# Kernel tuning notes

Measured on AMD Instinct MI355X. Metric: run time of the kernel, lower is better.

The kernel has to match this reference:

```python
import jax, jax.numpy as jnp
import numpy as np

B, P, F = 128, 4096, 32
K, D = 8, 64
ITERS = 2
EPS_ATTN = 1e-8
EPS_LN = 1e-5
SCALE = D ** -0.5


def _layernorm(x, g, b):
    mu = jnp.mean(x, axis=-1, keepdims=True)
    var = jnp.mean((x - mu) ** 2, axis=-1, keepdims=True)
    return (x - mu) * jax.lax.rsqrt(var + EPS_LN) * g + b


def setup_inputs() -> dict:
    key = jax.random.key(0)
    ks = jax.random.split(key, 16)
    s = lambda fan_in: 1.0 / np.sqrt(fan_in)
    inp = {
        "x": jax.random.normal(ks[0], (B, P, F), dtype=jnp.float32),
        "noise": jax.random.normal(ks[1], (B, K, D), dtype=jnp.float32),
        "slots_mu": jax.random.normal(ks[2], (1, 1, D), dtype=jnp.float32),
        "slots_sigma": jnp.ones((1, 1, D), dtype=jnp.float32) * 0.1,
        # torch Linear weights: [out, in]
        "Wq": jax.random.uniform(ks[3], (D, D), jnp.float32, -s(D), s(D)),
        "Wk": jax.random.uniform(ks[4], (D, F), jnp.float32, -s(F), s(F)),
        "Wv": jax.random.uniform(ks[5], (D, F), jnp.float32, -s(F), s(F)),
        # GRUCell params: weight_ih/[3D,D], weight_hh/[3D,D], biases [3D]
        "W_ih": jax.random.uniform(ks[6], (3 * D, D), jnp.float32, -s(D), s(D)),
        "W_hh": jax.random.uniform(ks[7], (3 * D, D), jnp.float32, -s(D), s(D)),
        "b_ih": jax.random.uniform(ks[8], (3 * D,), jnp.float32, -s(D), s(D)),
        "b_hh": jax.random.uniform(ks[9], (3 * D,), jnp.float32, -s(D), s(D)),
        "ln_in_g": jnp.ones((F,), jnp.float32),
        "ln_in_b": jnp.zeros((F,), jnp.float32),
        "ln_slots_g": jnp.ones((D,), jnp.float32),
        "ln_slots_b": jnp.zeros((D,), jnp.float32),
        "ff_ln_g": jnp.ones((D,), jnp.float32),
        "ff_ln_b": jnp.zeros((D,), jnp.float32),
        "ff_W1": jax.random.uniform(ks[10], (2 * D, D), jnp.float32, -s(D), s(D)),
        "ff_b1": jax.random.uniform(ks[11], (2 * D,), jnp.float32, -s(D), s(D)),
        "ff_W2": jax.random.uniform(ks[12], (D, 2 * D), jnp.float32, -s(2 * D), s(2 * D)),
        "ff_b2": jax.random.uniform(ks[13], (D,), jnp.float32, -s(2 * D), s(2 * D)),
    }
    return inp


def _gru_cell(x, h, W_ih, W_hh, b_ih, b_hh):
    # x, h: [N, D]
    gi = x @ W_ih.T + b_ih  # [N, 3D]
    gh = h @ W_hh.T + b_hh
    i_r, i_z, i_n = jnp.split(gi, 3, axis=-1)
    h_r, h_z, h_n = jnp.split(gh, 3, axis=-1)
    r = jax.nn.sigmoid(i_r + h_r)
    z = jax.nn.sigmoid(i_z + h_z)
    n = jnp.tanh(i_n + r * h_n)
    return (1.0 - z) * n + z * h


def reference(x, noise, slots_mu, slots_sigma, Wq, Wk, Wv, W_ih, W_hh, b_ih, b_hh,
              ln_in_g, ln_in_b, ln_slots_g, ln_slots_b,
              ff_ln_g, ff_ln_b, ff_W1, ff_b1, ff_W2, ff_b2):
    x_norm = _layernorm(x, ln_in_g, ln_in_b)          # [B,P,F]
    k = x_norm @ Wk.T                                  # [B,P,D]
    v = x_norm @ Wv.T                                  # [B,P,D]
    slots = slots_mu + jnp.abs(slots_sigma) * noise    # [B,K,D]
    last_attn = None
    for _ in range(ITERS):
        slots_prev = slots
        q = _layernorm(slots, ln_slots_g, ln_slots_b) @ Wq.T  # [B,K,D]
        dots = jnp.einsum('bkd,bpd->bkp', q, k) * SCALE       # [B,K,P]
        attn = jax.nn.softmax(dots, axis=1) + EPS_ATTN        # softmax over slots
        attn = attn / jnp.sum(attn, axis=-1, keepdims=True)   # normalize over pixels
        last_attn = attn
        updates = jnp.einsum('bkp,bpd->bkd', attn, v)         # [B,K,D]
        h = _gru_cell(updates.reshape(-1, D), slots_prev.reshape(-1, D),
                      W_ih, W_hh, b_ih, b_hh).reshape(x.shape[0], K, D)
        ff_in = _layernorm(h, ff_ln_g, ff_ln_b)
        ff_out = jax.nn.relu(ff_in @ ff_W1.T + ff_b1) @ ff_W2.T + ff_b2
        slots = h + ff_out
    return slots, last_attn
```

## Files before the change

### kernel.cpp

```cpp
#include <hip/hip_runtime.h>
#include <hip/hip_bf16.h>
#include <stdint.h>

#define Bb 128
#define Pp 4096
#define Ff 32
#define Kk 8
#define Dd 64

constexpr float EPS_ATTN_ = 1e-8f;
constexpr float EPS_LN_   = 1e-5f;
constexpr float SCALE_    = 0.125f;

typedef __attribute__((ext_vector_type(8))) short short8;
typedef __attribute__((ext_vector_type(4))) float floatx4;
typedef __attribute__((ext_vector_type(4))) unsigned uintx4;

__device__ __forceinline__ unsigned short f2bf(float f) {
  union { float f; unsigned u; } c; c.f = f;
  unsigned u = c.u + 0x7fffu + ((c.u >> 16) & 1u);
  return (unsigned short)(u >> 16);
}
__device__ __forceinline__ unsigned pkbf(float a, float b) {
  __hip_bfloat162 h2 = __float22bfloat162_rn(make_float2(a, b));
  union { __hip_bfloat162 h; unsigned u; } c; c.h = h2;
  return c.u;
}
__device__ __forceinline__ float wsum(float v) {
  v += __shfl_xor(v, 1, 64);  v += __shfl_xor(v, 2, 64);
  v += __shfl_xor(v, 4, 64);  v += __shfl_xor(v, 8, 64);
  v += __shfl_xor(v, 16, 64); v += __shfl_xor(v, 32, 64);
  return v;
}

__global__ __launch_bounds__(512) void init_kernel(
    const float* __restrict__ noise, const float* __restrict__ smu,
    const float* __restrict__ ssig, const float* __restrict__ Wq,
    const float* __restrict__ Wk,
    const float* __restrict__ lsg, const float* __restrict__ lsb,
    float* __restrict__ slots, unsigned short* __restrict__ qt_bf,
    float* __restrict__ acc_t, float* __restrict__ accs) {
  const int b = blockIdx.x;
  const int k = threadIdx.x >> 6;
  const int j = threadIdx.x & 63;
  __shared__ float lnv[Kk][Dd];
  __shared__ float wq[64 * 65];
  __shared__ float wk[64 * 33];
  {
    const float4* g4 = (const float4*)Wq;
    #pragma unroll
    for (int i = 0; i < 2; ++i) {
      int f4i = threadIdx.x + i * 512;
      float4 v = g4[f4i];
      int fi = f4i * 4, row = fi >> 6, col = fi & 63;
      float* dst = &wq[row * 65 + col];
      dst[0] = v.x; dst[1] = v.y; dst[2] = v.z; dst[3] = v.w;
    }
    const float4* gk = (const float4*)Wk;
    float4 v = gk[threadIdx.x];
    int fi = threadIdx.x * 4, row = fi >> 5, col = fi & 31;
    float* dst = &wk[row * 33 + col];
    dst[0] = v.x; dst[1] = v.y; dst[2] = v.z; dst[3] = v.w;
  }
  const size_t rk = (size_t)b * Kk + k;
  float s0 = smu[j] + fabsf(ssig[j]) * noise[rk * Dd + j];
  slots[rk * Dd + j] = s0;
  float mu  = wsum(s0) * (1.f / 64.f);
  float dc  = s0 - mu;
  float var = wsum(dc * dc) * (1.f / 64.f);
  float xn  = dc * rsqrtf(var + EPS_LN_) * lsg[j] + lsb[j];
  lnv[k][j] = xn;
  __syncthreads();
  float q = 0.f;
  #pragma unroll 8
  for (int d = 0; d < Dd; ++d) q = fmaf(wq[j * 65 + d], lnv[k][d], q);
  __syncthreads();
  lnv[k][j] = q * SCALE_;
  __syncthreads();
  if (j < Ff) {
    float qt = 0.f;
    #pragma unroll 8
    for (int d = 0; d < Dd; ++d) qt = fmaf(lnv[k][d], wk[d * 33 + j], qt);
    qt_bf[((size_t)b * 16 + k) * Ff + j]     = f2bf(qt);
    qt_bf[((size_t)b * 16 + k + 8) * Ff + j] = 0;
    acc_t[rk * Ff + j] = 0.f;
  }
  if (j == 0) accs[rk] = 0.f;
}

#define ROUNDS 2
template <bool LAST>
__global__ __launch_bounds__(256) void fattn_kernel(
    const float* __restrict__ x, const unsigned short* __restrict__ qt_bf,
    const float* __restrict__ lg, const float* __restrict__ lb,
    float* __restrict__ acc_t, float* __restrict__ accs,
    float* __restrict__ attn_out) {
  const int b  = blockIdx.x;
  const int w    = threadIdx.x >> 6;
  const int lane = threadIdx.x & 63;
  const int m    = lane & 15;
  const int quad = lane >> 4;
  __shared__ __align__(16) unsigned short xb[256 * 40];
  __shared__ __align__(16) unsigned short xbT[32 * 264];
  __shared__ __align__(16) unsigned short A_lds[4][8][72];

  const short8 aq = *(const short8*)(qt_bf + ((size_t)b * 16 + m) * Ff + quad * 8);

  float Ss0 = 0.f, Ss1 = 0.f, Ss2 = 0.f, Ss3 = 0.f;
  floatx4 Cg0 = {0.f,0.f,0.f,0.f}, Cg1 = {0.f,0.f,0.f,0.f};

  for (int rr = 0; rr < ROUNDS; ++rr) {
    const int p0 = (blockIdx.y * ROUNDS + rr) * 256;
    if (rr) __syncthreads();
    const float4* xp = (const float4*)(x + ((size_t)b * Pp + p0 + threadIdx.x) * Ff);
    float4 xr[8];
    #pragma unroll
    for (int i = 0; i < 8; ++i) xr[i] = xp[i];
    unsigned pku[16];
    {
      float xv[Ff];
      #pragma unroll
      for (int i = 0; i < 8; ++i) {
        xv[i*4] = xr[i].x; xv[i*4+1] = xr[i].y; xv[i*4+2] = xr[i].z; xv[i*4+3] = xr[i].w;
      }
      float mu = 0.f;
      #pragma unroll
      for (int j = 0; j < Ff; ++j) mu += xv[j];
      mu *= (1.f / Ff);
      float var = 0.f;
      #pragma unroll
      for (int j = 0; j < Ff; ++j) { float d = xv[j] - mu; var = fmaf(d, d, var); }
      var *= (1.f / Ff);
      float rn = rsqrtf(var + EPS_LN_);
      #pragma unroll
      for (int j = 0; j < Ff; ++j) xv[j] = (xv[j] - mu) * rn * lg[j] + lb[j];
      #pragma unroll
      for (int p = 0; p < 16; ++p) pku[p] = pkbf(xv[2 * p], xv[2 * p + 1]);
    }
    #pragma unroll
    for (int j8 = 0; j8 < 4; ++j8)
      *(uintx4*)&xb[threadIdx.x * 40 + j8 * 8] = *(uintx4*)&pku[j8 * 4];
    #pragma unroll
    for (int p = 0; p < 16; ++p) {
      xbT[(2 * p)     * 264 + threadIdx.x] = (unsigned short)(pku[p] & 0xffffu);
      xbT[(2 * p + 1) * 264 + threadIdx.x] = (unsigned short)(pku[p] >> 16);
    }
    __syncthreads();

    #pragma unroll
    for (int t = 0; t < 4; ++t) {
      const int lpx = w * 64 + t * 16 + m;
      const short8 bx = *(const short8*)&xb[lpx * 40 + quad * 8];
      floatx4 C = {0.f, 0.f, 0.f, 0.f};
      C = __builtin_amdgcn_mfma_f32_16x16x32_bf16(aq, bx, C, 0, 0, 0);
      float mx = fmaxf(fmaxf(C[0], C[1]), fmaxf(C[2], C[3]));
      mx = fmaxf(mx, __shfl_xor(mx, 16, 64));
      float e0 = __expf(C[0] - mx), e1 = __expf(C[1] - mx),
            e2 = __expf(C[2] - mx), e3 = __expf(C[3] - mx);
      float s = e0 + e1 + e2 + e3;
      s += __shfl_xor(s, 16, 64);
      float inv = 1.f / s;
      float a0 = fmaf(e0, inv, EPS_ATTN_), a1 = fmaf(e1, inv, EPS_ATTN_);
      float a2 = fmaf(e2, inv, EPS_ATTN_), a3 = fmaf(e3, inv, EPS_ATTN_);
      Ss0 += a0; Ss1 += a1; Ss2 += a2; Ss3 += a3;
      if (quad < 2) {
        const int r0 = quad * 4;
        unsigned c01 = pkbf(a0, a1), c23 = pkbf(a2, a3);
        A_lds[w][r0 + 0][t * 16 + m] = (unsigned short)(c01 & 0xffffu);
        A_lds[w][r0 + 1][t * 16 + m] = (unsigned short)(c01 >> 16);
        A_lds[w][r0 + 2][t * 16 + m] = (unsigned short)(c23 & 0xffffu);
        A_lds[w][r0 + 3][t * 16 + m] = (unsigned short)(c23 >> 16);
        if (LAST) {
          float* ao = attn_out + ((size_t)b * Kk + r0) * Pp + p0 + w * 64 + t * 16 + m;
          ao[0] = a0; ao[Pp] = a1; ao[2 * (size_t)Pp] = a2; ao[3 * (size_t)Pp] = a3;
        }
      }
    }
    __syncthreads();
    #pragma unroll
    for (int ks = 0; ks < 2; ++ks) {
      const short8 af = *(const short8*)(&A_lds[w][m & 7][ks * 32 + quad * 8]);
      const int pxo = w * 64 + ks * 32 + quad * 8;
      const short8 xg0 = *(const short8*)&xbT[(m)      * 264 + pxo];
      const short8 xg1 = *(const short8*)&xbT[(16 + m) * 264 + pxo];
      Cg0 = __builtin_amdgcn_mfma_f32_16x16x32_bf16(af, xg0, Cg0, 0, 0, 0);
      Cg1 = __builtin_amdgcn_mfma_f32_16x16x32_bf16(af, xg1, Cg1, 0, 0, 0);
    }
  }
  Ss0 += __shfl_xor(Ss0,1,64); Ss0 += __shfl_xor(Ss0,2,64); Ss0 += __shfl_xor(Ss0,4,64); Ss0 += __shfl_xor(Ss0,8,64);
  Ss1 += __shfl_xor(Ss1,1,64); Ss1 += __shfl_xor(Ss1,2,64); Ss1 += __shfl_xor(Ss1,4,64); Ss1 += __shfl_xor(Ss1,8,64);
  Ss2 += __shfl_xor(Ss2,1,64); Ss2 += __shfl_xor(Ss2,2,64); Ss2 += __shfl_xor(Ss2,4,64); Ss2 += __shfl_xor(Ss2,8,64);
  Ss3 += __shfl_xor(Ss3,1,64); Ss3 += __shfl_xor(Ss3,2,64); Ss3 += __shfl_xor(Ss3,4,64); Ss3 += __shfl_xor(Ss3,8,64);
  if (quad < 2) {
    const int row = quad * 4;
    float* tp = acc_t + ((size_t)b * Kk + row) * Ff + m;
    #pragma unroll
    for (int r = 0; r < 4; ++r) {
      atomicAdd(tp + (size_t)r * Ff,      Cg0[r]);
      atomicAdd(tp + (size_t)r * Ff + 16, Cg1[r]);
    }
    if (m == 0) {
      atomicAdd(&accs[b * Kk + row + 0], Ss0);
      atomicAdd(&accs[b * Kk + row + 1], Ss1);
      atomicAdd(&accs[b * Kk + row + 2], Ss2);
      atomicAdd(&accs[b * Kk + row + 3], Ss3);
    }
  }
}

template <bool LAST>
__global__ __launch_bounds__(256) void gru_kernel(
    const float* __restrict__ acc_t, const float* __restrict__ accs,
    float* __restrict__ slots,
    const float* __restrict__ W_ih, const float* __restrict__ W_hh,
    const float* __restrict__ b_ih, const float* __restrict__ b_hh,
    const float* __restrict__ fg, const float* __restrict__ fb,
    const float* __restrict__ W1, const float* __restrict__ b1,
    const float* __restrict__ W2, const float* __restrict__ b2,
    const float* __restrict__ lsg, const float* __restrict__ lsb,
    const float* __restrict__ Wq, const float* __restrict__ Wv,
    const float* __restrict__ Wk,
    unsigned short* __restrict__ qt_bf,
    float* __restrict__ acc_t2, float* __restrict__ accs2,
    float* __restrict__ out_slots) {
  const int b = blockIdx.x;
  const int kh = blockIdx.y;
  const int k = threadIdx.x >> 6;
  const int j = threadIdx.x & 63;
  const int kg = kh * 4 + k;
  __shared__ float WA[192 * 65];
  __shared__ float WB[192 * 65];
  __shared__ float WVs[64 * 33];
  __shared__ float WKs[64 * 33];
  __shared__ float At[4][Ff];
  __shared__ float Ub[4][Dd];
  __shared__ float Hb[4][Dd];
  __shared__ float Tb[4][2 * Dd];
  __shared__ float qs[4][Dd];
  {
    const float4* gi = (const float4*)W_ih;
    const float4* gh = (const float4*)W_hh;
    #pragma unroll
    for (int i = 0; i < 12; ++i) {
      int f4i = threadIdx.x + i * 256;
      float4 vi = gi[f4i], vh = gh[f4i];
      int fi = f4i * 4, row = fi >> 6, col = fi & 63;
      float* da = &WA[row * 65 + col];
      float* db = &WB[row * 65 + col];
      da[0]=vi.x; da[1]=vi.y; da[2]=vi.z; da[3]=vi.w;
      db[0]=vh.x; db[1]=vh.y; db[2]=vh.z; db[3]=vh.w;
    }
    const float4* gv = (const float4*)Wv;
    #pragma unroll
    for (int i = 0; i < 2; ++i) {
      int f4i = threadIdx.x + i * 256;
      float4 v = gv[f4i];
      int fi = f4i * 4, row = fi >> 5, col = fi & 31;
      float* d_ = &WVs[row * 33 + col];
      d_[0]=v.x; d_[1]=v.y; d_[2]=v.z; d_[3]=v.w;
    }
    if (!LAST) {
      const float4* gk = (const float4*)Wk;
      #pragma unroll
      for (int i = 0; i < 2; ++i) {
        int f4i = threadIdx.x + i * 256;
        float4 v = gk[f4i];
        int fi = f4i * 4, row = fi >> 5, col = fi & 31;
        float* d_ = &WKs[row * 33 + col];
        d_[0]=v.x; d_[1]=v.y; d_[2]=v.z; d_[3]=v.w;
      }
    }
  }
  const size_t rk = (size_t)b * Kk + kg;
  const float S = accs[rk];
  if (j < Ff) At[k][j] = acc_t[rk * Ff + j];
  const float h = slots[rk * Dd + j];
  Hb[k][j] = h;
  __syncthreads();
  float u = 0.f;
  #pragma unroll 8
  for (int f = 0; f < Ff; ++f) u = fmaf(WVs[j * 33 + f], At[k][f], u);
  u /= S;
  Ub[k][j] = u;
  __syncthreads();
  float gr = b_ih[j], gz = b_ih[64 + j], gn = b_ih[128 + j];
  float hr = b_hh[j], hz = b_hh[64 + j], hn_ = b_hh[128 + j];
  #pragma unroll 4
  for (int d = 0; d < Dd; ++d) {
    const float ud = Ub[k][d], hd = Hb[k][d];
    gr  = fmaf(WA[j * 65 + d],         ud, gr);
    gz  = fmaf(WA[(64 + j) * 65 + d],  ud, gz);
    gn  = fmaf(WA[(128 + j) * 65 + d], ud, gn);
    hr  = fmaf(WB[j * 65 + d],         hd, hr);
    hz  = fmaf(WB[(64 + j) * 65 + d],  hd, hz);
    hn_ = fmaf(WB[(128 + j) * 65 + d], hd, hn_);
  }
  const float r = 1.f / (1.f + __expf(-(gr + hr)));
  const float z = 1.f / (1.f + __expf(-(gz + hz)));
  const float n = tanhf(fmaf(r, hn_, gn));
  const float hnew = fmaf(z, h - n, n);
  float mu  = wsum(hnew) * (1.f / 64.f);
  float dc  = hnew - mu;
  float var = wsum(dc * dc) * (1.f / 64.f);
  float fi_ = dc * rsqrtf(var + EPS_LN_) * fg[j] + fb[j];
  __syncthreads();
  Ub[k][j] = fi_;
  {
    const float4* g1 = (const float4*)W1;
    #pragma unroll
    for (int i = 0; i < 8; ++i) {
      int f4i = threadIdx.x + i * 256;
      float4 v = g1[f4i];
      int fi = f4i * 4, row = fi >> 6, col = fi & 63;
      float* d_ = &WA[row * 65 + col];
      d_[0]=v.x; d_[1]=v.y; d_[2]=v.z; d_[3]=v.w;
    }
    if (!LAST) {
      const float4* gq = (const float4*)Wq;
      #pragma unroll
      for (int i = 0; i < 4; ++i) {
        int f4i = threadIdx.x + i * 256;
        float4 v = gq[f4i];
        int fi = f4i * 4, row = fi >> 6, col = fi & 63;
        float* d_ = &WA[8320 + row * 65 + col];
        d_[0]=v.x; d_[1]=v.y; d_[2]=v.z; d_[3]=v.w;
      }
    }
    const float4* g2 = (const float4*)W2;
    #pragma unroll
    for (int i = 0; i < 8; ++i) {
      int f4i = threadIdx.x + i * 256;
      float4 v = g2[f4i];
      int fi = f4i * 4, row = fi >> 7, col = fi & 127;
      float* d_ = &WB[row * 129 + col];
      d_[0]=v.x; d_[1]=v.y; d_[2]=v.z; d_[3]=v.w;
    }
  }
  __syncthreads();
  float f1a = b1[j], f1b = b1[64 + j];
  #pragma unroll 4
  for (int d = 0; d < Dd; ++d) {
    const float t = Ub[k][d];
    f1a = fmaf(WA[j * 65 + d],        t, f1a);
    f1b = fmaf(WA[(64 + j) * 65 + d], t, f1b);
  }
  f1a = fmaxf(f1a, 0.f);
  f1b = fmaxf(f1b, 0.f);
  Tb[k][j]      = f1a;
  Tb[k][64 + j] = f1b;
  __syncthreads();
  float o = b2[j];
  #pragma unroll 4
  for (int e = 0; e < 2 * Dd; ++e) o = fmaf(WB[j * 129 + e], Tb[k][e], o);
  const float sn = hnew + o;
  if (!LAST) {
    slots[rk * Dd + j] = sn;
    float mq = wsum(sn) * (1.f / 64.f);
    float dq = sn - mq;
    float vq = wsum(dq * dq) * (1.f / 64.f);
    float xq = dq * rsqrtf(vq + EPS_LN_) * lsg[j] + lsb[j];
    Ub[k][j] = xq;
    __syncthreads();
    float q = 0.f;
    #pragma unroll 8
    for (int d = 0; d < Dd; ++d) q = fmaf(WA[8320 + j * 65 + d], Ub[k][d], q);
    qs[k][j] = q * SCALE_;
    __syncthreads();
    if (j < Ff) {
      float qt = 0.f;
      #pragma unroll 8
      for (int d = 0; d < Dd; ++d) qt = fmaf(qs[k][d], WKs[d * 33 + j], qt);
      qt_bf[((size_t)b * 16 + kg) * Ff + j]     = f2bf(qt);
      qt_bf[((size_t)b * 16 + kg + 8) * Ff + j] = 0;
      acc_t2[rk * Ff + j] = 0.f;
    }
    if (j == 0) accs2[rk] = 0.f;
  } else {
    out_slots[rk * Dd + j] = sn;
  }
}

__global__ __launch_bounds__(256) void scale_kernel(
    const float* __restrict__ accs, float* __restrict__ attn) {
  const size_t idx = ((size_t)blockIdx.x * 256 + threadIdx.x) * 4;
  const int bk = (int)(idx >> 12);
  const float inv = 1.f / accs[bk];
  float4 v = *(float4*)(attn + idx);
  v.x *= inv; v.y *= inv; v.z *= inv; v.w *= inv;
  *(float4*)(attn + idx) = v;
}

extern "C" void kernel_launch(void* const* d_in, const int* in_sizes, int n_in,
                              void* d_out, int out_size, void* d_ws, size_t ws_size,
                              hipStream_t stream) {
  const float* x      = (const float*)d_in[0];
  const float* noise  = (const float*)d_in[1];
  const float* smu    = (const float*)d_in[2];
  const float* ssig   = (const float*)d_in[3];
  const float* Wq     = (const float*)d_in[4];
  const float* Wk     = (const float*)d_in[5];
  const float* Wv     = (const float*)d_in[6];
  const float* W_ih   = (const float*)d_in[7];
  const float* W_hh   = (const float*)d_in[8];
  const float* b_ih   = (const float*)d_in[9];
  const float* b_hh   = (const float*)d_in[10];
  const float* ln_in_g = (const float*)d_in[11];
  const float* ln_in_b = (const float*)d_in[12];
  const float* ln_s_g  = (const float*)d_in[13];
  const float* ln_s_b  = (const float*)d_in[14];
  const float* ff_g   = (const float*)d_in[15];
  const float* ff_b   = (const float*)d_in[16];
  const float* W1     = (const float*)d_in[17];
  const float* b1     = (const float*)d_in[18];
  const float* W2     = (const float*)d_in[19];
  const float* b2     = (const float*)d_in[20];

  char* ws = (char*)d_ws;
  unsigned short* qt_bf = (unsigned short*)(ws);
  float* slots  = (float*)(ws + 131072);
  float* acc_t1 = (float*)(ws + 393216);
  float* accs1  = (float*)(ws + 524288);
  float* acc_t2 = (float*)(ws + 528384);
  float* accs2  = (float*)(ws + 659456);

  float* out_slots = (float*)d_out;
  float* out_attn  = out_slots + (size_t)Bb * Kk * Dd;

  init_kernel<<<dim3(Bb), dim3(512), 0, stream>>>(
      noise, smu, ssig, Wq, Wk, ln_s_g, ln_s_b, slots, qt_bf, acc_t1, accs1);
  fattn_kernel<false><<<dim3(Bb, 16 / ROUNDS), dim3(256), 0, stream>>>(
      x, qt_bf, ln_in_g, ln_in_b, acc_t1, accs1, nullptr);
  gru_kernel<false><<<dim3(Bb, 2), dim3(256), 0, stream>>>(
      acc_t1, accs1, slots, W_ih, W_hh, b_ih, b_hh, ff_g, ff_b,
      W1, b1, W2, b2, ln_s_g, ln_s_b, Wq, Wv, Wk, qt_bf, acc_t2, accs2, nullptr);
  fattn_kernel<true><<<dim3(Bb, 16 / ROUNDS), dim3(256), 0, stream>>>(
      x, qt_bf, ln_in_g, ln_in_b, acc_t2, accs2, out_attn);
  gru_kernel<true><<<dim3(Bb, 2), dim3(256), 0, stream>>>(
      acc_t2, accs2, slots, W_ih, W_hh, b_ih, b_hh, ff_g, ff_b,
      W1, b1, W2, b2, ln_s_g, ln_s_b, Wq, Wv, Wk, qt_bf, acc_t2, accs2, out_slots);
  scale_kernel<<<dim3(4096), dim3(256), 0, stream>>>(accs2, out_attn);
}
```

Before: 202.9 us.

## Fuse init into first attention, replace atomics with partials, stage x via LDS

Drops the separate init kernel. The first attention kernel now builds the initial slots, q and qt itself, per block. Global atomicAdd accumulation becomes per-slice partial sums that the GRU and scale kernels reduce, which also removes the zeroing writes. x is loaded with coalesced float4 reads staged through LDS, and the intermediate attention map is stored as bf16 before final scaling to fp32. The trade-offs are redundant qt computation in every block, extra reduction loads, and reduced precision in the attention output.

```diff
diff --git a/kernel.cpp b/kernel.cpp
--- a/kernel.cpp
+++ b/kernel.cpp
@@ -21,6 +21,10 @@
   unsigned u = c.u + 0x7fffu + ((c.u >> 16) & 1u);
   return (unsigned short)(u >> 16);
 }
+__device__ __forceinline__ float bf2f(unsigned h) {
+  union { float f; unsigned u; } c; c.u = h << 16;
+  return c.f;
+}
 __device__ __forceinline__ unsigned pkbf(float a, float b) {
   __hip_bfloat162 h2 = __float22bfloat162_rn(make_float2(a, b));
   union { __hip_bfloat162 h; unsigned u; } c; c.h = h2;
@@ -33,78 +37,90 @@
   return v;
 }
 
-__global__ __launch_bounds__(512) void init_kernel(
-    const float* __restrict__ noise, const float* __restrict__ smu,
-    const float* __restrict__ ssig, const float* __restrict__ Wq,
-    const float* __restrict__ Wk,
-    const float* __restrict__ lsg, const float* __restrict__ lsb,
-    float* __restrict__ slots, unsigned short* __restrict__ qt_bf,
-    float* __restrict__ acc_t, float* __restrict__ accs) {
-  const int b = blockIdx.x;
-  const int k = threadIdx.x >> 6;
-  const int j = threadIdx.x & 63;
-  __shared__ float lnv[Kk][Dd];
-  __shared__ float wq[64 * 65];
-  __shared__ float wk[64 * 33];
-  {
-    const float4* g4 = (const float4*)Wq;
-    #pragma unroll
-    for (int i = 0; i < 2; ++i) {
-      int f4i = threadIdx.x + i * 512;
-      float4 v = g4[f4i];
-      int fi = f4i * 4, row = fi >> 6, col = fi & 63;
-      float* dst = &wq[row * 65 + col];
-      dst[0] = v.x; dst[1] = v.y; dst[2] = v.z; dst[3] = v.w;
-    }
-    const float4* gk = (const float4*)Wk;
-    float4 v = gk[threadIdx.x];
-    int fi = threadIdx.x * 4, row = fi >> 5, col = fi & 31;
-    float* dst = &wk[row * 33 + col];
-    dst[0] = v.x; dst[1] = v.y; dst[2] = v.z; dst[3] = v.w;
-  }
-  const size_t rk = (size_t)b * Kk + k;
-  float s0 = smu[j] + fabsf(ssig[j]) * noise[rk * Dd + j];
-  slots[rk * Dd + j] = s0;
-  float mu  = wsum(s0) * (1.f / 64.f);
-  float dc  = s0 - mu;
-  float var = wsum(dc * dc) * (1.f / 64.f);
-  float xn  = dc * rsqrtf(var + EPS_LN_) * lsg[j] + lsb[j];
-  lnv[k][j] = xn;
-  __syncthreads();
-  float q = 0.f;
-  #pragma unroll 8
-  for (int d = 0; d < Dd; ++d) q = fmaf(wq[j * 65 + d], lnv[k][d], q);
-  __syncthreads();
-  lnv[k][j] = q * SCALE_;
-  __syncthreads();
-  if (j < Ff) {
-    float qt = 0.f;
-    #pragma unroll 8
-    for (int d = 0; d < Dd; ++d) qt = fmaf(lnv[k][d], wk[d * 33 + j], qt);
-    qt_bf[((size_t)b * 16 + k) * Ff + j]     = f2bf(qt);
-    qt_bf[((size_t)b * 16 + k + 8) * Ff + j] = 0;
-    acc_t[rk * Ff + j] = 0.f;
-  }
-  if (j == 0) accs[rk] = 0.f;
-}
-
 #define ROUNDS 2
-template <bool LAST>
+template <bool FIRST>
 __global__ __launch_bounds__(256) void fattn_kernel(
     const float* __restrict__ x, const unsigned short* __restrict__ qt_bf,
     const float* __restrict__ lg, const float* __restrict__ lb,
-    float* __restrict__ acc_t, float* __restrict__ accs,
-    float* __restrict__ attn_out) {
+    const float* __restrict__ noise, const float* __restrict__ smu,
+    const float* __restrict__ ssig, const float* __restrict__ Wq,
+    const float* __restrict__ Wk, const float* __restrict__ lsg,
+    const float* __restrict__ lsb,
+    float* __restrict__ acc_tp, float* __restrict__ Ssp,
+    unsigned short* __restrict__ attn_bf) {
   const int b  = blockIdx.x;
   const int w    = threadIdx.x >> 6;
   const int lane = threadIdx.x & 63;
   const int m    = lane & 15;
   const int quad = lane >> 4;
-  __shared__ __align__(16) unsigned short xb[256 * 40];
-  __shared__ __align__(16) unsigned short xbT[32 * 264];
-  __shared__ __align__(16) unsigned short A_lds[4][8][72];
-
-  const short8 aq = *(const short8*)(qt_bf + ((size_t)b * 16 + m) * Ff + quad * 8);
+  __shared__ __align__(16) char smem[41984];
+  float* xs = (float*)smem;
+  unsigned short* xb  = (unsigned short*)smem;
+  unsigned short* xbT = (unsigned short*)(smem + 20480);
+  unsigned short (*A_lds)[8][72] = (unsigned short (*)[8][72])(smem + 37376);
+
+  short8 aq;
+  if (FIRST) {
+    float* wq  = (float*)smem;
+    float* wk  = (float*)(smem + 16640);
+    float* lnv = (float*)(smem + 25088);
+    unsigned short* qtb = (unsigned short*)(smem + 27136);
+    {
+      const float4* g4 = (const float4*)Wq;
+      #pragma unroll
+      for (int i = 0; i < 4; ++i) {
+        int f4i = threadIdx.x + i * 256;
+        float4 v = g4[f4i];
+        int fi = f4i * 4, row = fi >> 6, col = fi & 63;
+        float* dst = &wq[row * 65 + col];
+        dst[0] = v.x; dst[1] = v.y; dst[2] = v.z; dst[3] = v.w;
+      }
+      const float4* gk = (const float4*)Wk;
+      #pragma unroll
+      for (int i = 0; i < 2; ++i) {
+        int f4i = threadIdx.x + i * 256;
+        float4 v = gk[f4i];
+        int fi = f4i * 4, row = fi >> 5, col = fi & 31;
+        float* dst = &wk[row * 33 + col];
+        dst[0] = v.x; dst[1] = v.y; dst[2] = v.z; dst[3] = v.w;
+      }
+    }
+    const int j = lane;
+    #pragma unroll
+    for (int kk0 = 0; kk0 < 2; ++kk0) {
+      const int kk = w + kk0 * 4;
+      float s0 = smu[j] + fabsf(ssig[j]) * noise[((size_t)b * Kk + kk) * Dd + j];
+      float mu  = wsum(s0) * (1.f / 64.f);
+      float dc  = s0 - mu;
+      float var = wsum(dc * dc) * (1.f / 64.f);
+      lnv[kk * 64 + j] = dc * rsqrtf(var + EPS_LN_) * lsg[j] + lsb[j];
+    }
+    __syncthreads();
+    float qa = 0.f, qb = 0.f;
+    #pragma unroll 8
+    for (int d = 0; d < Dd; ++d) {
+      float wv = wq[j * 65 + d];
+      qa = fmaf(wv, lnv[w * 64 + d],       qa);
+      qb = fmaf(wv, lnv[(w + 4) * 64 + d], qb);
+    }
+    __syncthreads();
+    lnv[w * 64 + j]       = qa * SCALE_;
+    lnv[(w + 4) * 64 + j] = qb * SCALE_;
+    __syncthreads();
+    {
+      const int kq = threadIdx.x >> 5, fq = threadIdx.x & 31;
+      float qt = 0.f;
+      #pragma unroll 8
+      for (int d = 0; d < Dd; ++d) qt = fmaf(lnv[kq * 64 + d], wk[d * 33 + fq], qt);
+      qtb[kq * 32 + fq]       = f2bf(qt);
+      qtb[(kq + 8) * 32 + fq] = 0;
+    }
+    __syncthreads();
+    aq = *(const short8*)&qtb[m * 32 + quad * 8];
+    __syncthreads();
+  } else {
+    aq = *(const short8*)(qt_bf + ((size_t)b * 16 + m) * Ff + quad * 8);
+  }
 
   float Ss0 = 0.f, Ss1 = 0.f, Ss2 = 0.f, Ss3 = 0.f;
   floatx4 Cg0 = {0.f,0.f,0.f,0.f}, Cg1 = {0.f,0.f,0.f,0.f};
@@ -112,16 +128,26 @@
   for (int rr = 0; rr < ROUNDS; ++rr) {
     const int p0 = (blockIdx.y * ROUNDS + rr) * 256;
     if (rr) __syncthreads();
-    const float4* xp = (const float4*)(x + ((size_t)b * Pp + p0 + threadIdx.x) * Ff);
-    float4 xr[8];
-    #pragma unroll
-    for (int i = 0; i < 8; ++i) xr[i] = xp[i];
+    {
+      const float4* xg4 = (const float4*)(x + ((size_t)b * Pp + p0) * Ff);
+      float4 st[8];
+      #pragma unroll
+      for (int i = 0; i < 8; ++i) st[i] = xg4[threadIdx.x + i * 256];
+      #pragma unroll
+      for (int i = 0; i < 8; ++i) {
+        int f4i = threadIdx.x + i * 256;
+        int px = f4i >> 3, c = (f4i & 7) * 4;
+        *(float4*)&xs[px * 36 + c] = st[i];
+      }
+    }
+    __syncthreads();
     unsigned pku[16];
     {
       float xv[Ff];
       #pragma unroll
-      for (int i = 0; i < 8; ++i) {
-        xv[i*4] = xr[i].x; xv[i*4+1] = xr[i].y; xv[i*4+2] = xr[i].z; xv[i*4+3] = xr[i].w;
+      for (int j4 = 0; j4 < 8; ++j4) {
+        float4 t = *(const float4*)&xs[threadIdx.x * 36 + j4 * 4];
+        xv[j4*4] = t.x; xv[j4*4+1] = t.y; xv[j4*4+2] = t.z; xv[j4*4+3] = t.w;
       }
       float mu = 0.f;
       #pragma unroll
@@ -137,6 +163,7 @@
       #pragma unroll
       for (int p = 0; p < 16; ++p) pku[p] = pkbf(xv[2 * p], xv[2 * p + 1]);
     }
+    __syncthreads();
     #pragma unroll
     for (int j8 = 0; j8 < 4; ++j8)
       *(uintx4*)&xb[threadIdx.x * 40 + j8 * 8] = *(uintx4*)&pku[j8 * 4];
@@ -170,9 +197,12 @@
         A_lds[w][r0 + 1][t * 16 + m] = (unsigned short)(c01 >> 16);
         A_lds[w][r0 + 2][t * 16 + m] = (unsigned short)(c23 & 0xffffu);
         A_lds[w][r0 + 3][t * 16 + m] = (unsigned short)(c23 >> 16);
-        if (LAST) {
-          float* ao = attn_out + ((size_t)b * Kk + r0) * Pp + p0 + w * 64 + t * 16 + m;
-          ao[0] = a0; ao[Pp] = a1; ao[2 * (size_t)Pp] = a2; ao[3 * (size_t)Pp] = a3;
+        if (!FIRST) {
+          unsigned short* ao = attn_bf + ((size_t)b * Kk + r0) * Pp + p0 + w * 64 + t * 16 + m;
+          ao[0]      = (unsigned short)(c01 & 0xffffu);
+          ao[Pp]     = (unsigned short)(c01 >> 16);
+          ao[2 * Pp] = (unsigned short)(c23 & 0xffffu);
+          ao[3 * Pp] = (unsigned short)(c23 >> 16);
         }
       }
     }
@@ -193,25 +223,26 @@
   Ss3 += __shfl_xor(Ss3,1,64); Ss3 += __shfl_xor(Ss3,2,64); Ss3 += __shfl_xor(Ss3,4,64); Ss3 += __shfl_xor(Ss3,8,64);
   if (quad < 2) {
     const int row = quad * 4;
-    float* tp = acc_t + ((size_t)b * Kk + row) * Ff + m;
+    const int slice = blockIdx.y * 4 + w;
+    float* tp = acc_tp + (size_t)b * 8192 + (size_t)slice * 256 + (size_t)row * 32 + m;
     #pragma unroll
     for (int r = 0; r < 4; ++r) {
-      atomicAdd(tp + (size_t)r * Ff,      Cg0[r]);
-      atomicAdd(tp + (size_t)r * Ff + 16, Cg1[r]);
+      tp[r * 32]      = Cg0[r];
+      tp[r * 32 + 16] = Cg1[r];
     }
     if (m == 0) {
-      atomicAdd(&accs[b * Kk + row + 0], Ss0);
-      atomicAdd(&accs[b * Kk + row + 1], Ss1);
-      atomicAdd(&accs[b * Kk + row + 2], Ss2);
-      atomicAdd(&accs[b * Kk + row + 3], Ss3);
+      float* sp = Ssp + ((size_t)b * 32 + slice) * 8 + row;
+      sp[0] = Ss0; sp[1] = Ss1; sp[2] = Ss2; sp[3] = Ss3;
     }
   }
 }
 
 template <bool LAST>
 __global__ __launch_bounds__(256) void gru_kernel(
-    const float* __restrict__ acc_t, const float* __restrict__ accs,
+    const float* __restrict__ acc_tp, const float* __restrict__ Ssp,
     float* __restrict__ slots,
+    const float* __restrict__ noise, const float* __restrict__ smu,
+    const float* __restrict__ ssig,
     const float* __restrict__ W_ih, const float* __restrict__ W_hh,
     const float* __restrict__ b_ih, const float* __restrict__ b_hh,
     const float* __restrict__ fg, const float* __restrict__ fb,
@@ -221,7 +252,6 @@
     const float* __restrict__ Wq, const float* __restrict__ Wv,
     const float* __restrict__ Wk,
     unsigned short* __restrict__ qt_bf,
-    float* __restrict__ acc_t2, float* __restrict__ accs2,
     float* __restrict__ out_slots) {
   const int b = blockIdx.x;
   const int kh = blockIdx.y;
@@ -272,9 +302,19 @@
     }
   }
   const size_t rk = (size_t)b * Kk + kg;
-  const float S = accs[rk];
-  if (j < Ff) At[k][j] = acc_t[rk * Ff + j];
-  const float h = slots[rk * Dd + j];
+  float S = 0.f;
+  #pragma unroll
+  for (int y = 0; y < 32; ++y) S += Ssp[((size_t)b * 32 + y) * 8 + kg];
+  if (j < Ff) {
+    const float* tp = acc_tp + (size_t)b * 8192 + (size_t)kg * 32 + j;
+    float t = 0.f;
+    #pragma unroll
+    for (int y = 0; y < 32; ++y) t += tp[y * 256];
+    At[k][j] = t;
+  }
+  float h;
+  if (LAST) h = slots[rk * Dd + j];
+  else      h = smu[j] + fabsf(ssig[j]) * noise[rk * Dd + j];
   Hb[k][j] = h;
   __syncthreads();
   float u = 0.f;
@@ -372,22 +412,29 @@
       for (int d = 0; d < Dd; ++d) qt = fmaf(qs[k][d], WKs[d * 33 + j], qt);
       qt_bf[((size_t)b * 16 + kg) * Ff + j]     = f2bf(qt);
       qt_bf[((size_t)b * 16 + kg + 8) * Ff + j] = 0;
-      acc_t2[rk * Ff + j] = 0.f;
-    }
-    if (j == 0) accs2[rk] = 0.f;
+    }
   } else {
     out_slots[rk * Dd + j] = sn;
   }
 }
 
 __global__ __launch_bounds__(256) void scale_kernel(
-    const float* __restrict__ accs, float* __restrict__ attn) {
+    const float* __restrict__ Ssp, const unsigned short* __restrict__ attn_bf,
+    float* __restrict__ out_attn) {
   const size_t idx = ((size_t)blockIdx.x * 256 + threadIdx.x) * 4;
   const int bk = (int)(idx >> 12);
-  const float inv = 1.f / accs[bk];
-  float4 v = *(float4*)(attn + idx);
-  v.x *= inv; v.y *= inv; v.z *= inv; v.w *= inv;
-  *(float4*)(attn + idx) = v;
+  const int b = bk >> 3, k = bk & 7;
+  float S = 0.f;
+  #pragma unroll
+  for (int y = 0; y < 32; ++y) S += Ssp[((size_t)b * 32 + y) * 8 + k];
+  const float inv = 1.f / S;
+  uint2 v = *(const uint2*)(attn_bf + idx);
+  float4 o;
+  o.x = bf2f(v.x & 0xffffu) * inv;
+  o.y = bf2f(v.x >> 16)     * inv;
+  o.z = bf2f(v.y & 0xffffu) * inv;
+  o.w = bf2f(v.y >> 16)     * inv;
+  *(float4*)(out_attn + idx) = o;
 }
 
 extern "C" void kernel_launch(void* const* d_in, const int* in_sizes, int n_in,
@@ -417,26 +464,25 @@
 
   char* ws = (char*)d_ws;
   unsigned short* qt_bf = (unsigned short*)(ws);
-  float* slots  = (float*)(ws + 131072);
-  float* acc_t1 = (float*)(ws + 393216);
-  float* accs1  = (float*)(ws + 524288);
-  float* acc_t2 = (float*)(ws + 528384);
-  float* accs2  = (float*)(ws + 659456);
+  float* slots   = (float*)(ws + 131072);
+  float* acc_tp  = (float*)(ws + 393216);
+  float* Ssp     = (float*)(ws + 4587520);
+  unsigned short* attn_bf = (unsigned short*)(ws + 4718592);
 
   float* out_slots = (float*)d_out;
   float* out_attn  = out_slots + (size_t)Bb * Kk * Dd;
 
-  init_kernel<<<dim3(Bb), dim3(512), 0, stream>>>(
-      noise, smu, ssig, Wq, Wk, ln_s_g, ln_s_b, slots, qt_bf, acc_t1, accs1);
-  fattn_kernel<false><<<dim3(Bb, 16 / ROUNDS), dim3(256), 0, stream>>>(
-      x, qt_bf, ln_in_g, ln_in_b, acc_t1, accs1, nullptr);
+  fattn_kernel<true><<<dim3(Bb, 8), dim3(256), 0, stream>>>(
+      x, qt_bf, ln_in_g, ln_in_b, noise, smu, ssig, Wq, Wk, ln_s_g, ln_s_b,
+      acc_tp, Ssp, nullptr);
   gru_kernel<false><<<dim3(Bb, 2), dim3(256), 0, stream>>>(
-      acc_t1, accs1, slots, W_ih, W_hh, b_ih, b_hh, ff_g, ff_b,
-      W1, b1, W2, b2, ln_s_g, ln_s_b, Wq, Wv, Wk, qt_bf, acc_t2, accs2, nullptr);
-  fattn_kernel<true><<<dim3(Bb, 16 / ROUNDS), dim3(256), 0, stream>>>(
-      x, qt_bf, ln_in_g, ln_in_b, acc_t2, accs2, out_attn);
+      acc_tp, Ssp, slots, noise, smu, ssig, W_ih, W_hh, b_ih, b_hh, ff_g, ff_b,
+      W1, b1, W2, b2, ln_s_g, ln_s_b, Wq, Wv, Wk, qt_bf, nullptr);
+  fattn_kernel<false><<<dim3(Bb, 8), dim3(256), 0, stream>>>(
+      x, qt_bf, ln_in_g, ln_in_b, nullptr, nullptr, nullptr, nullptr, nullptr,
+      nullptr, nullptr, acc_tp, Ssp, attn_bf);
   gru_kernel<true><<<dim3(Bb, 2), dim3(256), 0, stream>>>(
-      acc_t2, accs2, slots, W_ih, W_hh, b_ih, b_hh, ff_g, ff_b,
-      W1, b1, W2, b2, ln_s_g, ln_s_b, Wq, Wv, Wk, qt_bf, acc_t2, accs2, out_slots);
-  scale_kernel<<<dim3(4096), dim3(256), 0, stream>>>(accs2, out_attn);
-}
+      acc_tp, Ssp, slots, noise, smu, ssig, W_ih, W_hh, b_ih, b_hh, ff_g, ff_b,
+      W1, b1, W2, b2, ln_s_g, ln_s_b, Wq, Wv, Wk, qt_bf, out_slots);
+  scale_kernel<<<dim3(4096), dim3(256), 0, stream>>>(Ssp, attn_bf, out_attn);
+}
```

Result: faster. 197.4 us (-2.7%).
